# Performance work log

Hardware: AMD Instinct MI355X
Metric: run time of the kernel (lower is better)

The kernel has to match this reference:

```python
import jax, jax.numpy as jnp
import numpy as np

D_MODEL = 1024
N_HEADS = 16
D_K = D_MODEL // N_HEADS
THETA = 10000.0
B, S = 2, 2048


def _rope(x):
    # x: [B, H, S, Dh], interleaved-pair RoPE with positions arange(S)
    Dh = x.shape[-1]
    inv_freq = 1.0 / (THETA ** (jnp.arange(0, Dh, 2, dtype=jnp.float32) / Dh))  # [Dh/2]
    pos = jnp.arange(x.shape[-2], dtype=jnp.float32)
    ang = pos[:, None] * inv_freq[None, :]                      # [S, Dh/2]
    cos = jnp.repeat(jnp.cos(ang), 2, axis=-1).astype(x.dtype)  # [S, Dh]
    sin = jnp.repeat(jnp.sin(ang), 2, axis=-1).astype(x.dtype)
    # rotate pairs: (x_2k, x_2k+1) -> (-x_2k+1, x_2k)
    xp = x.reshape(*x.shape[:-1], Dh // 2, 2)
    rot = jnp.stack((-xp[..., 1], xp[..., 0]), axis=-1).reshape(x.shape)
    return x * cos + rot * sin


def setup_inputs() -> dict:
    key = jax.random.key(0)
    ks = jax.random.split(key, 5)
    std = (2.0 / (D_MODEL + D_MODEL)) ** 0.5
    return {
        "x": jax.random.normal(ks[0], (B, S, D_MODEL), dtype=jnp.float32),
        "wq": jax.random.normal(ks[1], (D_MODEL, D_MODEL), dtype=jnp.float32) * std,
        "wk": jax.random.normal(ks[2], (D_MODEL, D_MODEL), dtype=jnp.float32) * std,
        "wv": jax.random.normal(ks[3], (D_MODEL, D_MODEL), dtype=jnp.float32) * std,
        "wo": jax.random.normal(ks[4], (D_MODEL, D_MODEL), dtype=jnp.float32) * std,
    }


def reference(x, wq, wk, wv, wo):
    b, s, _ = x.shape
    def split_heads(t):
        return t.reshape(b, s, N_HEADS, D_K).transpose(0, 2, 1, 3)  # [B,H,S,Dk]
    # Linear: y = x @ W.T  (weights stored [out, in])
    q = split_heads(jnp.einsum('bsd,od->bso', x, wq))
    k = split_heads(jnp.einsum('bsd,od->bso', x, wk))
    v = split_heads(jnp.einsum('bsd,od->bso', x, wv))
    q = _rope(q)
    k = _rope(k)
    scores = jnp.einsum('bhqd,bhkd->bhqk', q, k) / jnp.sqrt(jnp.asarray(D_K, x.dtype))
    causal = jnp.tril(jnp.ones((s, s), dtype=bool))
    scores = jnp.where(causal[None, None], scores, -jnp.inf)
    attn = jax.nn.softmax(scores, axis=-1)
    out = jnp.einsum('bhqk,bhkd->bhqd', attn, v)
    out = out.transpose(0, 2, 1, 3).reshape(b, s, D_MODEL)
    return jnp.einsum('bsd,od->bso', out, wo)
```

## Files before the change

### kernel.cpp

```cpp
#include <hip/hip_runtime.h>


typedef unsigned short u16;
typedef __attribute__((ext_vector_type(8))) short short8;
typedef __attribute__((ext_vector_type(4))) float float4v;

typedef const __attribute__((address_space(1))) void GV;
typedef __attribute__((address_space(3))) void LV;

#define VSTR 72
#define QSCL 0.18033688011112042f

__device__ __forceinline__ u16 f2b(float f) {
    union { float f; unsigned int i; } t; t.f = f;
    unsigned int r = t.i + 0x7fffu + ((t.i >> 16) & 1u);
    return (u16)(r >> 16);
}

__global__ __launch_bounds__(256) void cvt_all(
    const float4* __restrict__ x,  const float4* __restrict__ wq,
    const float4* __restrict__ wk, const float4* __restrict__ wv,
    const float4* __restrict__ wo,
    u16* __restrict__ xb, u16* __restrict__ wcat, u16* __restrict__ wob)
{
    const int i = blockIdx.x * 256 + threadIdx.x;
    const float4* s; u16* d; int off;
    if (i < 524288) { s = x; d = xb; off = i; }
    else {
        const int widx = i - 524288;
        const int w = widx >> 17, o = widx & 131071;
        switch (w) {
            case 0:  s = wq; d = wcat;              break;
            case 1:  s = wk; d = wcat + (1 << 20);  break;
            case 2:  s = wv; d = wcat + (2 << 20);  break;
            default: s = wo; d = wob;               break;
        }
        off = o;
    }
    float4 a = s[2 * off], b = s[2 * off + 1];
    u16 t[8] = {f2b(a.x), f2b(a.y), f2b(a.z), f2b(a.w),
                f2b(b.x), f2b(b.y), f2b(b.z), f2b(b.w)};
    reinterpret_cast<int4*>(d)[off] = *reinterpret_cast<int4*>(t);
}

__global__ __launch_bounds__(256) void rope_tab(float2* __restrict__ tab) {
    const int i = blockIdx.x * 256 + threadIdx.x;
    const int pos = i >> 5, fi = i & 31;
    const float freq = exp2f((float)fi * -0.4152410118609203f);
    float sn, cs; sincosf((float)pos * freq, &sn, &cs);
    tab[i] = make_float2(cs, sn);
}

template<int NT, int ROPE, int NBLK>
__global__ __launch_bounds__(256) void gemm_tile(
    const u16* __restrict__ X, const u16* __restrict__ Wb,
    u16* __restrict__ Yq, u16* __restrict__ Yk, u16* __restrict__ Yv,
    float* __restrict__ Yf, const float2* __restrict__ tab)
{
    __shared__ u16 As[128 * 64];
    __shared__ u16 Bs[NT * 32 * 64];

    const int tid  = threadIdx.x;
    const int wave = tid >> 6;
    const int lane = tid & 63;
    const int quad = lane >> 4;
    const int l16  = lane & 15;
    const int wm = (wave >> 1) * 64, wn = (wave & 1) * (NT * 16);
    const int g = blockIdx.x;
    const int rr = g >> 3;
    const int m0 = ((g & 7) * 4 + rr / NBLK) * 128;
    const int n0 = (rr % NBLK) * (NT * 32);
    const int lrow = lane >> 3;
    const int cg8  = (lane & 7) ^ lrow;

    float4v acc[4][NT];
#pragma unroll
    for (int mt = 0; mt < 4; mt++)
#pragma unroll
        for (int nt = 0; nt < NT; nt++) acc[mt][nt] = (float4v){0.f, 0.f, 0.f, 0.f};

    for (int kb = 0; kb < 1024; kb += 64) {
        __syncthreads();
#pragma unroll
        for (int t = 0; t < 4; t++) {
            const int I = wave * 4 + t;
            const u16* gp = X + (size_t)(m0 + I * 8 + lrow) * 1024 + kb + cg8 * 8;
            __builtin_amdgcn_global_load_lds((GV*)gp, (LV*)&As[I * 512], 16, 0, 0);
        }
#pragma unroll
        for (int t = 0; t < NT; t++) {
            const int I = wave * NT + t;
            const u16* gp = Wb + (size_t)(n0 + I * 8 + lrow) * 1024 + kb + cg8 * 8;
            __builtin_amdgcn_global_load_lds((GV*)gp, (LV*)&Bs[I * 512], 16, 0, 0);
        }
        __syncthreads();
#pragma unroll
        for (int ks = 0; ks < 2; ks++) {
            const int su = ((ks * 4 + quad) ^ (l16 & 7)) * 8;
            short8 af[4], bf[NT];
#pragma unroll
            for (int t = 0; t < 4; t++)
                af[t] = *reinterpret_cast<const short8*>(&As[(wm + t * 16 + l16) * 64 + su]);
#pragma unroll
            for (int t = 0; t < NT; t++)
                bf[t] = *reinterpret_cast<const short8*>(&Bs[(wn + t * 16 + l16) * 64 + su]);
#pragma unroll
            for (int mt = 0; mt < 4; mt++)
#pragma unroll
                for (int nt = 0; nt < NT; nt++)
                    acc[mt][nt] = __builtin_amdgcn_mfma_f32_16x16x32_bf16(af[mt], bf[nt], acc[mt][nt], 0, 0, 0);
        }
    }

    if (ROPE) {
#pragma unroll
        for (int nt = 0; nt < NT; nt++) {
            const int cg = n0 + wn + nt * 16 + l16;
            const int buf = cg >> 10;
            const int c = cg & 1023;
            u16* dst = (buf == 0) ? Yq : ((buf == 1) ? Yk : Yv);
            const bool rp = (buf < 2);
            const float scl = (buf == 0) ? QSCL : 1.0f;
            const int fi = (cg & 63) >> 1;
#pragma unroll
            for (int mt = 0; mt < 4; mt++)
#pragma unroll
                for (int r = 0; r < 4; r++) {
                    const int row = m0 + wm + mt * 16 + quad * 4 + r;
                    float v = acc[mt][nt][r];
                    if (rp) {
                        const float2 t = tab[((row & 2047) << 5) + fi];
                        const float partner = __shfl_xor(v, 1);
                        v = (l16 & 1) ? fmaf(v, t.x,  partner * t.y)
                                      : fmaf(v, t.x, -partner * t.y);
                    }
                    dst[(size_t)row * 1024 + c] = f2b(v * scl);
                }
        }
    } else {
#pragma unroll
        for (int nt = 0; nt < NT; nt++) {
            const int col = n0 + wn + nt * 16 + l16;
#pragma unroll
            for (int mt = 0; mt < 4; mt++)
#pragma unroll
                for (int r = 0; r < 4; r++) {
                    const int row = m0 + wm + mt * 16 + quad * 4 + r;
                    Yf[(size_t)row * 1024 + col] = acc[mt][nt][r];
                }
        }
    }
}

__global__ __launch_bounds__(256, 2) void attn_kernel(
    const u16* Q, const u16* __restrict__ K,
    const u16* __restrict__ V, u16* O)
{
    __shared__ u16 Vt[64 * VSTR];

    const int tid  = threadIdx.x;
    const int wave = tid >> 6;
    const int lane = tid & 63;
    const int quad = lane >> 4;
    const int l16  = lane & 15;
    const int g = blockIdx.x;
    const int xcd = g & 7, slot = g >> 3;
    const int G = (slot >> 4) * 8 + xcd;
    const int qtA = slot & 15;
    const int qtB = 31 - qtA;
    const int b = G & 1, h = G >> 1;
    const size_t base = ((size_t)b * 2048) * 1024 + (size_t)h * 64;

    short8 qfA[2], qfB[2];
    {
        const size_t ra = base + (size_t)(qtA * 64 + wave * 16 + l16) * 1024;
        qfA[0] = *reinterpret_cast<const short8*>(Q + ra + quad * 8);
        qfA[1] = *reinterpret_cast<const short8*>(Q + ra + 32 + quad * 8);
        const size_t rb = base + (size_t)(qtB * 64 + wave * 16 + l16) * 1024;
        qfB[0] = *reinterpret_cast<const short8*>(Q + rb + quad * 8);
        qfB[1] = *reinterpret_cast<const short8*>(Q + rb + 32 + quad * 8);
    }

    float4v oA[4], oB[4];
#pragma unroll
    for (int i = 0; i < 4; i++) { oA[i] = (float4v){0.f,0.f,0.f,0.f}; oB[i] = (float4v){0.f,0.f,0.f,0.f}; }
    float sA = 0.f, sB = 0.f;

    const int srow = tid >> 2;
    const int cb   = (tid & 3) << 4;
    const int sxw  = srow ^ cb;

    const u16* Vp = V + base + (size_t)srow * 1024 + cb;
    const u16* kbase = K + base + (size_t)l16 * 1024 + quad * 8;
    int4 vr0 = *reinterpret_cast<const int4*>(Vp);
    int4 vr1 = *reinterpret_cast<const int4*>(Vp + 8);
    short8 kn[4][2], kc[4][2], vf[4][2];
#pragma unroll
    for (int nt = 0; nt < 4; nt++)
#pragma unroll
        for (int ks = 0; ks < 2; ks++)
            kn[nt][ks] = *reinterpret_cast<const short8*>(kbase + (size_t)(nt * 16) * 1024 + ks * 32);

    const int bpa0 = (((quad & 1) * 2) * 16 + l16) * 4;
    const int bpa1 = bpa0 + 64;
    const bool hiq = quad >= 2;
    const int qloc = wave * 16 + l16;

    auto qk = [&](const short8 (&qf)[2], float4v (&sacc)[4]) {
#pragma unroll
        for (int nt = 0; nt < 4; nt++) {
            sacc[nt] = (float4v){0.f, 0.f, 0.f, 0.f};
#pragma unroll
            for (int ks = 0; ks < 2; ks++)
                sacc[nt] = __builtin_amdgcn_mfma_f32_16x16x32_bf16(kc[nt][ks], qf[ks], sacc[nt], 0, 0, 0);
        }
    };
    auto smx = [&](const float4v (&sacc)[4], float &sr, short8 (&pa)[2], bool diag) {
        unsigned int w[4][2];
#pragma unroll
        for (int nt = 0; nt < 4; nt++) {
            float p[4];
#pragma unroll
            for (int r = 0; r < 4; r++) {
                float sv = sacc[nt][r];
                if (diag && (nt * 16 + quad * 4 + r > qloc)) sv = -1e30f;
                p[r] = exp2f(sv);
                sr += p[r];
            }
            asm("v_cvt_pk_bf16_f32 %0, %1, %2" : "=v"(w[nt][0]) : "v"(p[0]), "v"(p[1]));
            asm("v_cvt_pk_bf16_f32 %0, %1, %2" : "=v"(w[nt][1]) : "v"(p[2]), "v"(p[3]));
        }
#pragma unroll
        for (int ks = 0; ks < 2; ks++) {
            unsigned int pw[4];
#pragma unroll
            for (int j = 0; j < 4; j++) {
                const int addr = (j >> 1) ? bpa1 : bpa0;
                const int rp = j & 1;
                int lo_ = __builtin_amdgcn_ds_bpermute(addr, (int)w[2 * ks][rp]);
                int hi_ = __builtin_amdgcn_ds_bpermute(addr, (int)w[2 * ks + 1][rp]);
                pw[j] = (unsigned int)(hiq ? hi_ : lo_);
            }
            union { unsigned int u[4]; short8 s; } t;
            t.u[0] = pw[0]; t.u[1] = pw[1]; t.u[2] = pw[2]; t.u[3] = pw[3];
            pa[ks] = t.s;
        }
    };
    auto pv = [&](const short8 (&pa)[2], float4v (&oc)[4]) {
#pragma unroll
        for (int ks = 0; ks < 2; ks++)
#pragma unroll
            for (int dt = 0; dt < 4; dt++)
                oc[dt] = __builtin_amdgcn_mfma_f32_16x16x32_bf16(pa[ks], vf[dt][ks], oc[dt], 0, 0, 0);
    };

    for (int j = 0; j <= qtB; j++) {
        __syncthreads();
        {
            const u16* a = reinterpret_cast<const u16*>(&vr0);
            const u16* c = reinterpret_cast<const u16*>(&vr1);
#pragma unroll
            for (int e = 0; e < 8; e++) Vt[(cb + e) * VSTR + sxw] = a[e];
#pragma unroll
            for (int e = 0; e < 8; e++) Vt[(cb + 8 + e) * VSTR + sxw] = c[e];
        }
#pragma unroll
        for (int nt = 0; nt < 4; nt++)
#pragma unroll
            for (int ks = 0; ks < 2; ks++) kc[nt][ks] = kn[nt][ks];
        __syncthreads();
        if (j < qtB) {
            Vp += 65536;
            vr0 = *reinterpret_cast<const int4*>(Vp);
            vr1 = *reinterpret_cast<const int4*>(Vp + 8);
            const u16* kb2 = kbase + (size_t)(j + 1) * 65536;
#pragma unroll
            for (int nt = 0; nt < 4; nt++)
#pragma unroll
                for (int ks = 0; ks < 2; ks++)
                    kn[nt][ks] = *reinterpret_cast<const short8*>(kb2 + (size_t)(nt * 16) * 1024 + ks * 32);
        }
#pragma unroll
        for (int nt = 0; nt < 4; nt++)
#pragma unroll
            for (int ks = 0; ks < 2; ks++)
                vf[nt][ks] = *reinterpret_cast<const short8*>(&Vt[(nt * 16 + l16) * VSTR + ((ks * 32 + quad * 8) ^ (nt << 4))]);

        if (j <= qtA) {
            float4v xA[4], xB[4];
            qk(qfA, xA);
            qk(qfB, xB);
            short8 paA[2], paB[2];
            smx(xA, sA, paA, j == qtA);
            smx(xB, sB, paB, false);
            pv(paA, oA);
            pv(paB, oB);
        } else {
            float4v xB[4];
            qk(qfB, xB);
            short8 paB[2];
            smx(xB, sB, paB, j == qtB);
            pv(paB, oB);
        }
    }

    float tA = sA, tB = sB;
    tA += __shfl_xor(tA, 16); tA += __shfl_xor(tA, 32);
    tB += __shfl_xor(tB, 16); tB += __shfl_xor(tB, 32);
#pragma unroll
    for (int r = 0; r < 4; r++) {
        const int rl = quad * 4 + r;
        const float invA = 1.0f / __shfl(tA, rl);
        const float invB = 1.0f / __shfl(tB, rl);
        const size_t rowA = base + (size_t)(qtA * 64 + wave * 16 + rl) * 1024;
        const size_t rowB = base + (size_t)(qtB * 64 + wave * 16 + rl) * 1024;
#pragma unroll
        for (int dt = 0; dt < 4; dt++) {
            O[rowA + dt * 16 + l16] = f2b(oA[dt][r] * invA);
            O[rowB + dt * 16 + l16] = f2b(oB[dt][r] * invB);
        }
    }
}

extern "C" void kernel_launch(void* const* d_in, const int* in_sizes, int n_in,
                              void* d_out, int out_size, void* d_ws, size_t ws_size,
                              hipStream_t stream) {
    (void)in_sizes; (void)n_in; (void)out_size; (void)ws_size;
    const float* x  = (const float*)d_in[0];
    const float* wq = (const float*)d_in[1];
    const float* wk = (const float*)d_in[2];
    const float* wv = (const float*)d_in[3];
    const float* wo = (const float*)d_in[4];

    const size_t MN = (size_t)4096 * 1024;

    u16* xb   = (u16*)d_out;
    u16* wcat = xb + MN;
    float2* tab = (float2*)(wcat + (size_t)3072 * 1024);
    u16* qbuf = (u16*)d_ws;
    u16* kbuf = qbuf + MN;
    u16* vbuf = kbuf + MN;
    u16* wob  = vbuf + MN;

    cvt_all<<<4096, 256, 0, stream>>>((const float4*)x, (const float4*)wq,
                                      (const float4*)wk, (const float4*)wv,
                                      (const float4*)wo, xb, wcat, wob);
    rope_tab<<<256, 256, 0, stream>>>(tab);
    gemm_tile<4, 1, 24><<<768, 256, 0, stream>>>(xb, wcat, qbuf, kbuf, vbuf, nullptr, tab);
    attn_kernel<<<512, 256, 0, stream>>>(qbuf, kbuf, vbuf, qbuf);
    gemm_tile<2, 0, 16><<<512, 256, 0, stream>>>(qbuf, wob, nullptr, nullptr, nullptr, (float*)d_out, nullptr);
}
```

Baseline: 228.0 us.

## Split attention work across two wave groups with balanced key-tile loop

```diff
diff --git a/kernel.cpp b/kernel.cpp
--- a/kernel.cpp
+++ b/kernel.cpp
@@ -152,14 +152,19 @@
     }
 }
 
-__global__ __launch_bounds__(256, 2) void attn_kernel(
+__global__ __launch_bounds__(512, 4) void attn_kernel(
     const u16* Q, const u16* __restrict__ K,
     const u16* __restrict__ V, u16* O)
 {
-    __shared__ u16 Vt[64 * VSTR];
+    __shared__ union {
+        u16 vt[2][64 * VSTR];
+        struct { float o[4][64][17]; float s[4][64]; } m;
+    } sm;
 
     const int tid  = threadIdx.x;
     const int wave = tid >> 6;
+    const int grp  = wave >> 2;
+    const int w4   = wave & 3;
     const int lane = tid & 63;
     const int quad = lane >> 4;
     const int l16  = lane & 15;
@@ -171,153 +176,170 @@
     const int b = G & 1, h = G >> 1;
     const size_t base = ((size_t)b * 2048) * 1024 + (size_t)h * 64;
 
-    short8 qfA[2], qfB[2];
+    int myqt = grp ? qtB : qtA;
+    short8 qf[2];
     {
-        const size_t ra = base + (size_t)(qtA * 64 + wave * 16 + l16) * 1024;
-        qfA[0] = *reinterpret_cast<const short8*>(Q + ra + quad * 8);
-        qfA[1] = *reinterpret_cast<const short8*>(Q + ra + 32 + quad * 8);
-        const size_t rb = base + (size_t)(qtB * 64 + wave * 16 + l16) * 1024;
-        qfB[0] = *reinterpret_cast<const short8*>(Q + rb + quad * 8);
-        qfB[1] = *reinterpret_cast<const short8*>(Q + rb + 32 + quad * 8);
-    }
-
-    float4v oA[4], oB[4];
-#pragma unroll
-    for (int i = 0; i < 4; i++) { oA[i] = (float4v){0.f,0.f,0.f,0.f}; oB[i] = (float4v){0.f,0.f,0.f,0.f}; }
-    float sA = 0.f, sB = 0.f;
-
-    const int srow = tid >> 2;
-    const int cb   = (tid & 3) << 4;
-    const int sxw  = srow ^ cb;
-
-    const u16* Vp = V + base + (size_t)srow * 1024 + cb;
+        const size_t r = base + (size_t)(myqt * 64 + w4 * 16 + l16) * 1024;
+        qf[0] = *reinterpret_cast<const short8*>(Q + r + quad * 8);
+        qf[1] = *reinterpret_cast<const short8*>(Q + r + 32 + quad * 8);
+    }
+
+    float4v o[4];
+#pragma unroll
+    for (int i = 0; i < 4; i++) o[i] = (float4v){0.f,0.f,0.f,0.f};
+    float s = 0.f;
+
+    const int srow = tid >> 3;
+    const int c0   = (tid & 7) << 3;
+    const int sxw  = srow ^ ((c0 >> 4) << 4);
+
+    const u16* Vbase = V + base + (size_t)srow * 1024 + c0;
     const u16* kbase = K + base + (size_t)l16 * 1024 + quad * 8;
-    int4 vr0 = *reinterpret_cast<const int4*>(Vp);
-    int4 vr1 = *reinterpret_cast<const int4*>(Vp + 8);
-    short8 kn[4][2], kc[4][2], vf[4][2];
-#pragma unroll
-    for (int nt = 0; nt < 4; nt++)
-#pragma unroll
-        for (int ks = 0; ks < 2; ks++)
-            kn[nt][ks] = *reinterpret_cast<const short8*>(kbase + (size_t)(nt * 16) * 1024 + ks * 32);
+    int4 vrA = *reinterpret_cast<const int4*>(Vbase);
+    int4 vrB;
 
     const int bpa0 = (((quad & 1) * 2) * 16 + l16) * 4;
     const int bpa1 = bpa0 + 64;
     const bool hiq = quad >= 2;
-    const int qloc = wave * 16 + l16;
-
-    auto qk = [&](const short8 (&qf)[2], float4v (&sacc)[4]) {
-#pragma unroll
-        for (int nt = 0; nt < 4; nt++) {
-            sacc[nt] = (float4v){0.f, 0.f, 0.f, 0.f};
-#pragma unroll
-            for (int ks = 0; ks < 2; ks++)
-                sacc[nt] = __builtin_amdgcn_mfma_f32_16x16x32_bf16(kc[nt][ks], qf[ks], sacc[nt], 0, 0, 0);
-        }
-    };
-    auto smx = [&](const float4v (&sacc)[4], float &sr, short8 (&pa)[2], bool diag) {
-        unsigned int w[4][2];
-#pragma unroll
-        for (int nt = 0; nt < 4; nt++) {
-            float p[4];
+    const int qloc = w4 * 16 + l16;
+
+    for (int i = 0; i <= 16; ++i) {
+        const int tb = (i <= qtA) ? i : i + 16 - qtA;
+
+        if (grp == 0 && i == qtA + 1) {
+            float t = s;
+            t += __shfl_xor(t, 16); t += __shfl_xor(t, 32);
 #pragma unroll
             for (int r = 0; r < 4; r++) {
-                float sv = sacc[nt][r];
-                if (diag && (nt * 16 + quad * 4 + r > qloc)) sv = -1e30f;
-                p[r] = exp2f(sv);
-                sr += p[r];
-            }
-            asm("v_cvt_pk_bf16_f32 %0, %1, %2" : "=v"(w[nt][0]) : "v"(p[0]), "v"(p[1]));
-            asm("v_cvt_pk_bf16_f32 %0, %1, %2" : "=v"(w[nt][1]) : "v"(p[2]), "v"(p[3]));
-        }
-#pragma unroll
-        for (int ks = 0; ks < 2; ks++) {
-            unsigned int pw[4];
-#pragma unroll
-            for (int j = 0; j < 4; j++) {
-                const int addr = (j >> 1) ? bpa1 : bpa0;
-                const int rp = j & 1;
-                int lo_ = __builtin_amdgcn_ds_bpermute(addr, (int)w[2 * ks][rp]);
-                int hi_ = __builtin_amdgcn_ds_bpermute(addr, (int)w[2 * ks + 1][rp]);
-                pw[j] = (unsigned int)(hiq ? hi_ : lo_);
-            }
-            union { unsigned int u[4]; short8 s; } t;
-            t.u[0] = pw[0]; t.u[1] = pw[1]; t.u[2] = pw[2]; t.u[3] = pw[3];
-            pa[ks] = t.s;
-        }
-    };
-    auto pv = [&](const short8 (&pa)[2], float4v (&oc)[4]) {
-#pragma unroll
-        for (int ks = 0; ks < 2; ks++)
-#pragma unroll
-            for (int dt = 0; dt < 4; dt++)
-                oc[dt] = __builtin_amdgcn_mfma_f32_16x16x32_bf16(pa[ks], vf[dt][ks], oc[dt], 0, 0, 0);
-    };
-
-    for (int j = 0; j <= qtB; j++) {
+                const int rl = quad * 4 + r;
+                const float inv = 1.0f / __shfl(t, rl);
+                const size_t row = base + (size_t)(qtA * 64 + w4 * 16 + rl) * 1024;
+#pragma unroll
+                for (int dt = 0; dt < 4; dt++)
+                    O[row + dt * 16 + l16] = f2b(o[dt][r] * inv);
+            }
+#pragma unroll
+            for (int k = 0; k < 4; k++) o[k] = (float4v){0.f,0.f,0.f,0.f};
+            s = 0.f;
+            myqt = qtB;
+            const size_t r = base + (size_t)(qtB * 64 + w4 * 16 + l16) * 1024;
+            qf[0] = *reinterpret_cast<const short8*>(Q + r + quad * 8);
+            qf[1] = *reinterpret_cast<const short8*>(Q + r + 32 + quad * 8);
+        }
+
+        const int mytile = grp ? tb : i;
+        const bool active = (grp == 0) || (tb <= qtB);
+
+        short8 kc[4][2];
+        if (active) {
+            const u16* kp = kbase + (size_t)mytile * 65536;
+#pragma unroll
+            for (int nt = 0; nt < 4; nt++)
+#pragma unroll
+                for (int ks = 0; ks < 2; ks++)
+                    kc[nt][ks] = *reinterpret_cast<const short8*>(kp + (size_t)(nt * 16) * 1024 + ks * 32);
+        }
+
         __syncthreads();
         {
-            const u16* a = reinterpret_cast<const u16*>(&vr0);
-            const u16* c = reinterpret_cast<const u16*>(&vr1);
-#pragma unroll
-            for (int e = 0; e < 8; e++) Vt[(cb + e) * VSTR + sxw] = a[e];
-#pragma unroll
-            for (int e = 0; e < 8; e++) Vt[(cb + 8 + e) * VSTR + sxw] = c[e];
-        }
-#pragma unroll
-        for (int nt = 0; nt < 4; nt++)
-#pragma unroll
-            for (int ks = 0; ks < 2; ks++) kc[nt][ks] = kn[nt][ks];
+            const u16* a = reinterpret_cast<const u16*>(&vrA);
+#pragma unroll
+            for (int e = 0; e < 8; e++) sm.vt[0][(c0 + e) * VSTR + sxw] = a[e];
+        }
+        if (i > qtA && tb <= qtB) {
+            const u16* a = reinterpret_cast<const u16*>(&vrB);
+#pragma unroll
+            for (int e = 0; e < 8; e++) sm.vt[1][(c0 + e) * VSTR + sxw] = a[e];
+        }
         __syncthreads();
-        if (j < qtB) {
-            Vp += 65536;
-            vr0 = *reinterpret_cast<const int4*>(Vp);
-            vr1 = *reinterpret_cast<const int4*>(Vp + 8);
-            const u16* kb2 = kbase + (size_t)(j + 1) * 65536;
-#pragma unroll
-            for (int nt = 0; nt < 4; nt++)
+
+        if (i < 16) {
+            vrA = *reinterpret_cast<const int4*>(Vbase + (size_t)(i + 1) * 65536);
+            if (i + 1 > qtA) {
+                const int tbn = i + 17 - qtA;
+                if (tbn <= qtB)
+                    vrB = *reinterpret_cast<const int4*>(Vbase + (size_t)tbn * 65536);
+            }
+        }
+
+        if (active) {
+            const u16* Vt = sm.vt[(grp && i > qtA) ? 1 : 0];
+            float4v sacc[4];
+#pragma unroll
+            for (int nt = 0; nt < 4; nt++) {
+                sacc[nt] = (float4v){0.f, 0.f, 0.f, 0.f};
 #pragma unroll
                 for (int ks = 0; ks < 2; ks++)
-                    kn[nt][ks] = *reinterpret_cast<const short8*>(kb2 + (size_t)(nt * 16) * 1024 + ks * 32);
-        }
-#pragma unroll
-        for (int nt = 0; nt < 4; nt++)
-#pragma unroll
-            for (int ks = 0; ks < 2; ks++)
-                vf[nt][ks] = *reinterpret_cast<const short8*>(&Vt[(nt * 16 + l16) * VSTR + ((ks * 32 + quad * 8) ^ (nt << 4))]);
-
-        if (j <= qtA) {
-            float4v xA[4], xB[4];
-            qk(qfA, xA);
-            qk(qfB, xB);
-            short8 paA[2], paB[2];
-            smx(xA, sA, paA, j == qtA);
-            smx(xB, sB, paB, false);
-            pv(paA, oA);
-            pv(paB, oB);
-        } else {
-            float4v xB[4];
-            qk(qfB, xB);
-            short8 paB[2];
-            smx(xB, sB, paB, j == qtB);
-            pv(paB, oB);
-        }
-    }
-
-    float tA = sA, tB = sB;
-    tA += __shfl_xor(tA, 16); tA += __shfl_xor(tA, 32);
-    tB += __shfl_xor(tB, 16); tB += __shfl_xor(tB, 32);
-#pragma unroll
-    for (int r = 0; r < 4; r++) {
-        const int rl = quad * 4 + r;
-        const float invA = 1.0f / __shfl(tA, rl);
-        const float invB = 1.0f / __shfl(tB, rl);
-        const size_t rowA = base + (size_t)(qtA * 64 + wave * 16 + rl) * 1024;
-        const size_t rowB = base + (size_t)(qtB * 64 + wave * 16 + rl) * 1024;
-#pragma unroll
-        for (int dt = 0; dt < 4; dt++) {
-            O[rowA + dt * 16 + l16] = f2b(oA[dt][r] * invA);
-            O[rowB + dt * 16 + l16] = f2b(oB[dt][r] * invB);
+                    sacc[nt] = __builtin_amdgcn_mfma_f32_16x16x32_bf16(kc[nt][ks], qf[ks], sacc[nt], 0, 0, 0);
+            }
+            const bool diag = (mytile == myqt);
+            unsigned int w[4][2];
+#pragma unroll
+            for (int nt = 0; nt < 4; nt++) {
+                float p[4];
+#pragma unroll
+                for (int r = 0; r < 4; r++) {
+                    float sv = sacc[nt][r];
+                    if (diag && (nt * 16 + quad * 4 + r > qloc)) sv = -1e30f;
+                    p[r] = exp2f(sv);
+                    s += p[r];
+                }
+                asm("v_cvt_pk_bf16_f32 %0, %1, %2" : "=v"(w[nt][0]) : "v"(p[0]), "v"(p[1]));
+                asm("v_cvt_pk_bf16_f32 %0, %1, %2" : "=v"(w[nt][1]) : "v"(p[2]), "v"(p[3]));
+            }
+            short8 pa[2];
+#pragma unroll
+            for (int ks = 0; ks < 2; ks++) {
+                unsigned int pw[4];
+#pragma unroll
+                for (int j = 0; j < 4; j++) {
+                    const int addr = (j >> 1) ? bpa1 : bpa0;
+                    const int rp = j & 1;
+                    int lo_ = __builtin_amdgcn_ds_bpermute(addr, (int)w[2 * ks][rp]);
+                    int hi_ = __builtin_amdgcn_ds_bpermute(addr, (int)w[2 * ks + 1][rp]);
+                    pw[j] = (unsigned int)(hiq ? hi_ : lo_);
+                }
+                union { unsigned int u[4]; short8 s8; } t;
+                t.u[0] = pw[0]; t.u[1] = pw[1]; t.u[2] = pw[2]; t.u[3] = pw[3];
+                pa[ks] = t.s8;
+            }
+#pragma unroll
+            for (int ks = 0; ks < 2; ks++) {
+                short8 vfk[4];
+#pragma unroll
+                for (int dt = 0; dt < 4; dt++)
+                    vfk[dt] = *reinterpret_cast<const short8*>(&Vt[(dt * 16 + l16) * VSTR + ((ks * 32 + quad * 8) ^ (dt << 4))]);
+#pragma unroll
+                for (int dt = 0; dt < 4; dt++)
+                    o[dt] = __builtin_amdgcn_mfma_f32_16x16x32_bf16(pa[ks], vfk[dt], o[dt], 0, 0, 0);
+            }
+        }
+    }
+
+    __syncthreads();
+    if (grp == 0) {
+#pragma unroll
+        for (int dt = 0; dt < 4; dt++)
+#pragma unroll
+            for (int r = 0; r < 4; r++) sm.m.o[w4][lane][dt * 4 + r] = o[dt][r];
+        sm.m.s[w4][lane] = s;
+    }
+    __syncthreads();
+    if (grp == 1) {
+        float t = s + sm.m.s[w4][lane];
+#pragma unroll
+        for (int dt = 0; dt < 4; dt++)
+#pragma unroll
+            for (int r = 0; r < 4; r++) o[dt][r] += sm.m.o[w4][lane][dt * 4 + r];
+        t += __shfl_xor(t, 16); t += __shfl_xor(t, 32);
+#pragma unroll
+        for (int r = 0; r < 4; r++) {
+            const int rl = quad * 4 + r;
+            const float inv = 1.0f / __shfl(t, rl);
+            const size_t row = base + (size_t)(qtB * 64 + w4 * 16 + rl) * 1024;
+#pragma unroll
+            for (int dt = 0; dt < 4; dt++)
+                O[row + dt * 16 + l16] = f2b(o[dt][r] * inv);
         }
     }
 }
@@ -347,6 +369,6 @@
                                       (const float4*)wo, xb, wcat, wob);
     rope_tab<<<256, 256, 0, stream>>>(tab);
     gemm_tile<4, 1, 24><<<768, 256, 0, stream>>>(xb, wcat, qbuf, kbuf, vbuf, nullptr, tab);
-    attn_kernel<<<512, 256, 0, stream>>>(qbuf, kbuf, vbuf, qbuf);
+    attn_kernel<<<512, 512, 0, stream>>>(qbuf, kbuf, vbuf, qbuf);
     gemm_tile<2, 0, 16><<<512, 256, 0, stream>>>(qbuf, wob, nullptr, nullptr, nullptr, (float*)d_out, nullptr);
 }
```

After: 243.2 us. +6.7%, slower.

## Double-buffer V tile in LDS and drop bpermute via matching V fragment layout

Applied to the files above, without the earlier changes.

```diff
diff --git a/kernel.cpp b/kernel.cpp
--- a/kernel.cpp
+++ b/kernel.cpp
@@ -156,7 +156,7 @@
     const u16* Q, const u16* __restrict__ K,
     const u16* __restrict__ V, u16* O)
 {
-    __shared__ u16 Vt[64 * VSTR];
+    __shared__ __align__(16) u16 Vt[2][64 * VSTR];
 
     const int tid  = threadIdx.x;
     const int wave = tid >> 6;
@@ -201,9 +201,17 @@
         for (int ks = 0; ks < 2; ks++)
             kn[nt][ks] = *reinterpret_cast<const short8*>(kbase + (size_t)(nt * 16) * 1024 + ks * 32);
 
-    const int bpa0 = (((quad & 1) * 2) * 16 + l16) * 4;
-    const int bpa1 = bpa0 + 64;
-    const bool hiq = quad >= 2;
+    {
+        const u16* a = reinterpret_cast<const u16*>(&vr0);
+        const u16* c = reinterpret_cast<const u16*>(&vr1);
+#pragma unroll
+        for (int e = 0; e < 8; e++) Vt[0][(cb + e) * VSTR + sxw] = a[e];
+#pragma unroll
+        for (int e = 0; e < 8; e++) Vt[0][(cb + 8 + e) * VSTR + sxw] = c[e];
+    }
+    vr0 = *reinterpret_cast<const int4*>(Vp + 65536);
+    vr1 = *reinterpret_cast<const int4*>(Vp + 65536 + 8);
+
     const int qloc = wave * 16 + l16;
 
     auto qk = [&](const short8 (&qf)[2], float4v (&sacc)[4]) {
@@ -230,21 +238,11 @@
             asm("v_cvt_pk_bf16_f32 %0, %1, %2" : "=v"(w[nt][0]) : "v"(p[0]), "v"(p[1]));
             asm("v_cvt_pk_bf16_f32 %0, %1, %2" : "=v"(w[nt][1]) : "v"(p[2]), "v"(p[3]));
         }
-#pragma unroll
-        for (int ks = 0; ks < 2; ks++) {
-            unsigned int pw[4];
-#pragma unroll
-            for (int j = 0; j < 4; j++) {
-                const int addr = (j >> 1) ? bpa1 : bpa0;
-                const int rp = j & 1;
-                int lo_ = __builtin_amdgcn_ds_bpermute(addr, (int)w[2 * ks][rp]);
-                int hi_ = __builtin_amdgcn_ds_bpermute(addr, (int)w[2 * ks + 1][rp]);
-                pw[j] = (unsigned int)(hiq ? hi_ : lo_);
-            }
-            union { unsigned int u[4]; short8 s; } t;
-            t.u[0] = pw[0]; t.u[1] = pw[1]; t.u[2] = pw[2]; t.u[3] = pw[3];
-            pa[ks] = t.s;
-        }
+        union { unsigned int u[4]; short8 s8; } t;
+        t.u[0] = w[0][0]; t.u[1] = w[0][1]; t.u[2] = w[1][0]; t.u[3] = w[1][1];
+        pa[0] = t.s8;
+        t.u[0] = w[2][0]; t.u[1] = w[2][1]; t.u[2] = w[3][0]; t.u[3] = w[3][1];
+        pa[1] = t.s8;
     };
     auto pv = [&](const short8 (&pa)[2], float4v (&oc)[4]) {
 #pragma unroll
@@ -256,23 +254,24 @@
 
     for (int j = 0; j <= qtB; j++) {
         __syncthreads();
-        {
+        if (j < qtB) {
+            u16* D = Vt[(j + 1) & 1];
             const u16* a = reinterpret_cast<const u16*>(&vr0);
             const u16* c = reinterpret_cast<const u16*>(&vr1);
 #pragma unroll
-            for (int e = 0; e < 8; e++) Vt[(cb + e) * VSTR + sxw] = a[e];
-#pragma unroll
-            for (int e = 0; e < 8; e++) Vt[(cb + 8 + e) * VSTR + sxw] = c[e];
+            for (int e = 0; e < 8; e++) D[(cb + e) * VSTR + sxw] = a[e];
+#pragma unroll
+            for (int e = 0; e < 8; e++) D[(cb + 8 + e) * VSTR + sxw] = c[e];
         }
 #pragma unroll
         for (int nt = 0; nt < 4; nt++)
 #pragma unroll
             for (int ks = 0; ks < 2; ks++) kc[nt][ks] = kn[nt][ks];
-        __syncthreads();
         if (j < qtB) {
-            Vp += 65536;
-            vr0 = *reinterpret_cast<const int4*>(Vp);
-            vr1 = *reinterpret_cast<const int4*>(Vp + 8);
+            if (j + 2 <= qtB) {
+                vr0 = *reinterpret_cast<const int4*>(Vp + (size_t)(j + 2) * 65536);
+                vr1 = *reinterpret_cast<const int4*>(Vp + (size_t)(j + 2) * 65536 + 8);
+            }
             const u16* kb2 = kbase + (size_t)(j + 1) * 65536;
 #pragma unroll
             for (int nt = 0; nt < 4; nt++)
@@ -280,11 +279,22 @@
                 for (int ks = 0; ks < 2; ks++)
                     kn[nt][ks] = *reinterpret_cast<const short8*>(kb2 + (size_t)(nt * 16) * 1024 + ks * 32);
         }
-#pragma unroll
-        for (int nt = 0; nt < 4; nt++)
-#pragma unroll
-            for (int ks = 0; ks < 2; ks++)
-                vf[nt][ks] = *reinterpret_cast<const short8*>(&Vt[(nt * 16 + l16) * VSTR + ((ks * 32 + quad * 8) ^ (nt << 4))]);
+        {
+            const u16* B = Vt[j & 1];
+#pragma unroll
+            for (int dt = 0; dt < 4; dt++) {
+                const int rb = (dt * 16 + l16) * VSTR;
+#pragma unroll
+                for (int ks = 0; ks < 2; ks++) {
+                    const int k1 = (ks * 32 + quad * 4) ^ (dt << 4);
+                    const int k2 = (ks * 32 + 16 + quad * 4) ^ (dt << 4);
+                    union { struct { uint2 lo, hi; } p; short8 s8; } u;
+                    u.p.lo = *reinterpret_cast<const uint2*>(&B[rb + k1]);
+                    u.p.hi = *reinterpret_cast<const uint2*>(&B[rb + k2]);
+                    vf[dt][ks] = u.s8;
+                }
+            }
+        }
 
         if (j <= qtA) {
             float4v xA[4], xB[4];
```

New measurement: 229.5 us. Within noise of the previous version (+0.6%).
